# Performance work log

Measured on AMD Instinct MI355X. Metric: run time of the kernel, lower is better.

The kernel has to match this reference:

```python
import jax, jax.numpy as jnp
import numpy as np

N_NODES = 50000
N_EDGES = 800000
N_GRAPHS = 64
IN_CH = 64
HID = 64


def _gcn(x, W, b, src, dst, norm, self_norm, n):
    # GCNConv with self-loops and symmetric normalization (PyG defaults)
    h = x @ W  # [N, H]
    agg = jax.ops.segment_sum(norm[:, None] * h[src], dst, num_segments=n)
    return agg + self_norm[:, None] * h + b


def setup_inputs() -> dict:
    key = jax.random.key(0)
    ks = jax.random.split(key, 20)
    s = 0.1
    d = {
        'x': jax.random.normal(ks[0], (N_NODES, IN_CH), jnp.float32),
        'x_SC': jax.random.normal(ks[1], (N_NODES, IN_CH), jnp.float32),
        'W1': jax.random.normal(ks[2], (IN_CH, HID), jnp.float32) * s,
        'b1': jax.random.normal(ks[3], (HID,), jnp.float32) * s,
        'W2': jax.random.normal(ks[4], (HID, HID), jnp.float32) * s,
        'b2': jax.random.normal(ks[5], (HID,), jnp.float32) * s,
        'We': jax.random.normal(ks[6], (IN_CH, HID), jnp.float32) * s,
        'be': jax.random.normal(ks[7], (HID,), jnp.float32) * s,
        'W1s': jax.random.normal(ks[8], (IN_CH, HID), jnp.float32) * s,
        'b1s': jax.random.normal(ks[9], (HID,), jnp.float32) * s,
        'W2s': jax.random.normal(ks[10], (HID, HID), jnp.float32) * s,
        'b2s': jax.random.normal(ks[11], (HID,), jnp.float32) * s,
        'Wes': jax.random.normal(ks[12], (IN_CH, HID), jnp.float32) * s,
        'bes': jax.random.normal(ks[13], (HID,), jnp.float32) * s,
        'Wf': jax.random.normal(ks[14], (HID, 1), jnp.float32) * s,
        'bf': jax.random.normal(ks[15], (1,), jnp.float32) * s,
        'edge_index': jax.random.randint(ks[16], (2, N_EDGES), 0, N_NODES, jnp.int32),
        'batch': jnp.sort(jax.random.randint(ks[17], (N_NODES,), 0, N_GRAPHS, jnp.int32)),
        'num_graphs': N_GRAPHS,
    }
    return d


def reference(x, x_SC, W1, b1, W2, b2, We, be, W1s, b1s, W2s, b2s, Wes, bes, Wf, bf, edge_index, batch, num_graphs):
    n = x.shape[0]
    src, dst = edge_index[0], edge_index[1]
    # degree with self-loops (edge weight 1)
    deg = jnp.ones((n,), x.dtype).at[dst].add(jnp.ones((src.shape[0],), x.dtype))
    dinv = deg ** -0.5
    norm = dinv[src] * dinv[dst]
    self_norm = dinv * dinv

    h = jax.nn.relu(_gcn(x, W1, b1, src, dst, norm, self_norm, n)) + jax.nn.relu(x @ We + be)
    h = jax.nn.relu(_gcn(h, W2, b2, src, dst, norm, self_norm, n)) + h

    hs = jax.nn.relu(_gcn(x_SC, W1s, b1s, src, dst, norm, self_norm, n)) + jax.nn.relu(x_SC @ Wes + bes)
    hs = jax.nn.relu(_gcn(hs, W2s, b2s, src, dst, norm, self_norm, n)) + hs

    h = h + hs
    sums = jax.ops.segment_sum(h, batch, num_segments=num_graphs)
    cnts = jax.ops.segment_sum(jnp.ones((n,), h.dtype), batch, num_segments=num_graphs)
    pooled = sums / jnp.maximum(cnts, 1.0)[:, None]
    return pooled @ Wf + bf
```

## Files before the change

kernel.cpp:

```cpp
#include <hip/hip_runtime.h>
#include <stdint.h>


typedef _Float16 f16;
typedef _Float16 f16x2 __attribute__((ext_vector_type(2)));
typedef _Float16 f16x8 __attribute__((ext_vector_type(8)));
typedef float f32x4 __attribute__((ext_vector_type(4)));

__global__ void deg_count_k(const int* __restrict__ dst, int nE, int* __restrict__ cnt) {
    int i = blockIdx.x * blockDim.x + threadIdx.x;
    if (i < nE) atomicAdd(&cnt[dst[i]], 1);
}

__global__ void dinv_k(const int* __restrict__ cnt, int n, float* __restrict__ dinv) {
    int i = blockIdx.x * blockDim.x + threadIdx.x;
    if (i < n) dinv[i] = 1.0f / sqrtf(1.0f + (float)cnt[i]);
}

__global__ __launch_bounds__(256) void scanA_k(const int* __restrict__ cnt, int n,
                                               int* __restrict__ offs, int* __restrict__ bsums) {
    int tid = threadIdx.x, lane = tid & 63, wid = tid >> 6;
    int base = blockIdx.x * 1024 + tid * 4;
    int v0 = (base + 0 < n) ? cnt[base + 0] : 0;
    int v1 = (base + 1 < n) ? cnt[base + 1] : 0;
    int v2 = (base + 2 < n) ? cnt[base + 2] : 0;
    int v3 = (base + 3 < n) ? cnt[base + 3] : 0;
    int lsum = v0 + v1 + v2 + v3;
    int s = lsum;
#pragma unroll
    for (int off = 1; off < 64; off <<= 1) {
        int t = __shfl_up(s, off);
        if (lane >= off) s += t;
    }
    __shared__ int wt[4];
    if (lane == 63) wt[wid] = s;
    __syncthreads();
    int woff = 0;
    for (int w = 0; w < wid; ++w) woff += wt[w];
    int excl = woff + s - lsum;
    if (base + 0 < n) offs[base + 0] = excl;
    if (base + 1 < n) offs[base + 1] = excl + v0;
    if (base + 2 < n) offs[base + 2] = excl + v0 + v1;
    if (base + 3 < n) offs[base + 3] = excl + v0 + v1 + v2;
    if (tid == 0) bsums[blockIdx.x] = wt[0] + wt[1] + wt[2] + wt[3];
}

__global__ void scanB_k(const int* __restrict__ bsums, int nb, int* __restrict__ boffs) {
    int lane = threadIdx.x;
    int carry = 0;
    for (int base = 0; base < nb; base += 64) {
        int i = base + lane;
        int v = (i < nb) ? bsums[i] : 0;
        int s = v;
#pragma unroll
        for (int off = 1; off < 64; off <<= 1) {
            int t = __shfl_up(s, off);
            if (lane >= off) s += t;
        }
        if (i < nb) boffs[i] = carry + s - v;
        carry += __shfl(s, 63);
    }
}

__global__ __launch_bounds__(256) void scanC_k(int* __restrict__ offs,
                                               const int* __restrict__ boffs,
                                               int* __restrict__ cur, int n, int nE) {
    int boff = boffs[blockIdx.x];
    int base = blockIdx.x * 1024 + threadIdx.x * 4;
#pragma unroll
    for (int j = 0; j < 4; ++j) {
        int i = base + j;
        if (i < n) {
            int o = offs[i] + boff;
            offs[i] = o;
            cur[i] = o;
        }
    }
    if (blockIdx.x == 0 && threadIdx.x == 0) offs[n] = nE;
}

__global__ void fill_k(const int* __restrict__ src, const int* __restrict__ dst, int nE,
                       int* __restrict__ cur, int* __restrict__ elist) {
    int e = blockIdx.x * blockDim.x + threadIdx.x;
    if (e < nE) {
        int p = atomicAdd(&cur[dst[e]], 1);
        elist[p] = src[e];
    }
}

template <int NW, bool F16IN>
__global__ __launch_bounds__(256) void mm_mfma_k(
    const void* __restrict__ X1, const void* __restrict__ X2,
    const float* __restrict__ Wa1, const float* __restrict__ Wa2,
    const float* __restrict__ Wc1, const float* __restrict__ Wc2,
    const float* __restrict__ dinv,
    f16* __restrict__ Oa1, f16* __restrict__ Oa2,
    f16* __restrict__ Oc1, f16* __restrict__ Oc2,
    int xP, int oP, int n) {
    const int branch = blockIdx.y;
    const void* X   = branch ? X2 : X1;
    const float* Wa = branch ? Wa2 : Wa1;
    const float* Wc = branch ? Wc2 : Wc1;
    f16* Oa = branch ? Oa2 : Oa1;
    f16* Oc = branch ? Oc2 : Oc1;

    const int lane = threadIdx.x & 63;
    const int col = lane & 15;
    const int kgrp = lane >> 4;

    f16x8 wa[4][2], wc[4][2];
#pragma unroll
    for (int ct = 0; ct < 4; ++ct)
#pragma unroll
        for (int kk = 0; kk < 2; ++kk) {
#pragma unroll
            for (int j = 0; j < 8; ++j) {
                int widx = (kk * 32 + kgrp * 8 + j) * 64 + ct * 16 + col;
                wa[ct][kk][j] = (f16)Wa[widx];
                if (NW == 2) wc[ct][kk][j] = (f16)Wc[widx];
            }
        }

    const int wid = blockIdx.x * 4 + (threadIdx.x >> 6);
    const int nwaves = gridDim.x * 4;
    const int ntiles = (n + 15) >> 4;
    for (int t = wid; t < ntiles; t += nwaves) {
        int arow = t * 16 + col;
        if (arow >= n) arow = n - 1;
        f16x8 af[2];
#pragma unroll
        for (int kk = 0; kk < 2; ++kk) {
            if (F16IN) {
                af[kk] = *(const f16x8*)((const f16*)X + (size_t)arow * xP + kk * 32 + kgrp * 8);
            } else {
                const float4* px = (const float4*)((const float*)X + (size_t)arow * xP + kk * 32 + kgrp * 8);
                float4 u0 = px[0], u1 = px[1];
                af[kk][0] = (f16)u0.x; af[kk][1] = (f16)u0.y;
                af[kk][2] = (f16)u0.z; af[kk][3] = (f16)u0.w;
                af[kk][4] = (f16)u1.x; af[kk][5] = (f16)u1.y;
                af[kk][6] = (f16)u1.z; af[kk][7] = (f16)u1.w;
            }
        }
        f32x4 acca[4], accc[4];
#pragma unroll
        for (int ct = 0; ct < 4; ++ct) {
            acca[ct] = (f32x4)(0.0f);
            if (NW == 2) accc[ct] = (f32x4)(0.0f);
        }
#pragma unroll
        for (int ct = 0; ct < 4; ++ct)
#pragma unroll
            for (int kk = 0; kk < 2; ++kk) {
                acca[ct] = __builtin_amdgcn_mfma_f32_16x16x32_f16(af[kk], wa[ct][kk], acca[ct], 0, 0, 0);
                if (NW == 2)
                    accc[ct] = __builtin_amdgcn_mfma_f32_16x16x32_f16(af[kk], wc[ct][kk], accc[ct], 0, 0, 0);
            }
        int rbase = t * 16 + kgrp * 4;
#pragma unroll
        for (int j = 0; j < 4; ++j) {
            int row = rbase + j;
            if (row < n) {
                float d = dinv[row];
#pragma unroll
                for (int ct = 0; ct < 4; ++ct) {
                    Oa[(size_t)row * oP + ct * 16 + col] = (f16)(d * acca[ct][j]);
                    if (NW == 2)
                        Oc[(size_t)row * oP + ct * 16 + col] = (f16)(accc[ct][j]);
                }
            }
        }
    }
}

__global__ __launch_bounds__(256) void agg1_k(
    const int* __restrict__ offs, const int* __restrict__ elist,
    const uint32_t* __restrict__ Aw, const uint32_t* __restrict__ Sw,
    const float* __restrict__ b1, const float* __restrict__ b1s,
    const float* __restrict__ be, const float* __restrict__ bes,
    const float* __restrict__ dinv, uint32_t* __restrict__ Hw, int n) {
    int node = blockIdx.x * 4 + (threadIdx.x >> 6);
    int lane = threadIdx.x & 63;
    if (node >= n) return;
    int br = lane >> 5;
    int ch0 = (lane & 31) * 2;
    float bb0 = br ? b1s[ch0] : b1[ch0];
    float bb1 = br ? b1s[ch0 + 1] : b1[ch0 + 1];
    float bs0 = br ? bes[ch0] : be[ch0];
    float bs1 = br ? bes[ch0 + 1] : be[ch0 + 1];

    int e0 = offs[node], e1 = offs[node + 1];
    f16x2 selfv = __builtin_bit_cast(f16x2, Aw[(size_t)node * 64 + lane]);
    float acc0 = (float)selfv.x, acc1 = (float)selfv.y;
    int e = e0;
    for (; e + 7 < e1; e += 8) {
        int s0 = elist[e], s1 = elist[e + 1], s2 = elist[e + 2], s3 = elist[e + 3];
        int s4 = elist[e + 4], s5 = elist[e + 5], s6 = elist[e + 6], s7 = elist[e + 7];
        f16x2 v0 = __builtin_bit_cast(f16x2, Aw[(size_t)s0 * 64 + lane]);
        f16x2 v1 = __builtin_bit_cast(f16x2, Aw[(size_t)s1 * 64 + lane]);
        f16x2 v2 = __builtin_bit_cast(f16x2, Aw[(size_t)s2 * 64 + lane]);
        f16x2 v3 = __builtin_bit_cast(f16x2, Aw[(size_t)s3 * 64 + lane]);
        f16x2 v4 = __builtin_bit_cast(f16x2, Aw[(size_t)s4 * 64 + lane]);
        f16x2 v5 = __builtin_bit_cast(f16x2, Aw[(size_t)s5 * 64 + lane]);
        f16x2 v6 = __builtin_bit_cast(f16x2, Aw[(size_t)s6 * 64 + lane]);
        f16x2 v7 = __builtin_bit_cast(f16x2, Aw[(size_t)s7 * 64 + lane]);
        acc0 += (((float)v0.x + (float)v1.x) + ((float)v2.x + (float)v3.x)) +
                (((float)v4.x + (float)v5.x) + ((float)v6.x + (float)v7.x));
        acc1 += (((float)v0.y + (float)v1.y) + ((float)v2.y + (float)v3.y)) +
                (((float)v4.y + (float)v5.y) + ((float)v6.y + (float)v7.y));
    }
    for (; e < e1; ++e) {
        f16x2 v = __builtin_bit_cast(f16x2, Aw[(size_t)elist[e] * 64 + lane]);
        acc0 += (float)v.x;
        acc1 += (float)v.y;
    }
    float d = dinv[node];
    float g0 = fmaxf(d * acc0 + bb0, 0.0f);
    float g1 = fmaxf(d * acc1 + bb1, 0.0f);
    f16x2 sv = __builtin_bit_cast(f16x2, Sw[(size_t)node * 64 + lane]);
    g0 += fmaxf((float)sv.x + bs0, 0.0f);
    g1 += fmaxf((float)sv.y + bs1, 0.0f);
    f16x2 o; o.x = (f16)g0; o.y = (f16)g1;
    Hw[(size_t)node * 64 + lane] = __builtin_bit_cast(uint32_t, o);
}

__global__ __launch_bounds__(256) void agg2_dot_k(
    const int* __restrict__ offs, const int* __restrict__ elist,
    const uint32_t* __restrict__ Aw, const uint32_t* __restrict__ Hw,
    const float* __restrict__ b2, const float* __restrict__ b2s,
    const float* __restrict__ Wf, const float* __restrict__ dinv,
    float* __restrict__ dot, int n) {
    int node = blockIdx.x * 4 + (threadIdx.x >> 6);
    int lane = threadIdx.x & 63;
    if (node >= n) return;
    int br = lane >> 5;
    int ch0 = (lane & 31) * 2;
    float bb0 = br ? b2s[ch0] : b2[ch0];
    float bb1 = br ? b2s[ch0 + 1] : b2[ch0 + 1];
    float wf0 = Wf[ch0], wf1 = Wf[ch0 + 1];

    int e0 = offs[node], e1 = offs[node + 1];
    f16x2 selfv = __builtin_bit_cast(f16x2, Aw[(size_t)node * 64 + lane]);
    float acc0 = (float)selfv.x, acc1 = (float)selfv.y;
    int e = e0;
    for (; e + 7 < e1; e += 8) {
        int s0 = elist[e], s1 = elist[e + 1], s2 = elist[e + 2], s3 = elist[e + 3];
        int s4 = elist[e + 4], s5 = elist[e + 5], s6 = elist[e + 6], s7 = elist[e + 7];
        f16x2 v0 = __builtin_bit_cast(f16x2, Aw[(size_t)s0 * 64 + lane]);
        f16x2 v1 = __builtin_bit_cast(f16x2, Aw[(size_t)s1 * 64 + lane]);
        f16x2 v2 = __builtin_bit_cast(f16x2, Aw[(size_t)s2 * 64 + lane]);
        f16x2 v3 = __builtin_bit_cast(f16x2, Aw[(size_t)s3 * 64 + lane]);
        f16x2 v4 = __builtin_bit_cast(f16x2, Aw[(size_t)s4 * 64 + lane]);
        f16x2 v5 = __builtin_bit_cast(f16x2, Aw[(size_t)s5 * 64 + lane]);
        f16x2 v6 = __builtin_bit_cast(f16x2, Aw[(size_t)s6 * 64 + lane]);
        f16x2 v7 = __builtin_bit_cast(f16x2, Aw[(size_t)s7 * 64 + lane]);
        acc0 += (((float)v0.x + (float)v1.x) + ((float)v2.x + (float)v3.x)) +
                (((float)v4.x + (float)v5.x) + ((float)v6.x + (float)v7.x));
        acc1 += (((float)v0.y + (float)v1.y) + ((float)v2.y + (float)v3.y)) +
                (((float)v4.y + (float)v5.y) + ((float)v6.y + (float)v7.y));
    }
    for (; e < e1; ++e) {
        f16x2 v = __builtin_bit_cast(f16x2, Aw[(size_t)elist[e] * 64 + lane]);
        acc0 += (float)v.x;
        acc1 += (float)v.y;
    }
    float d = dinv[node];
    f16x2 hv = __builtin_bit_cast(f16x2, Hw[(size_t)node * 64 + lane]);
    float h0 = fmaxf(d * acc0 + bb0, 0.0f) + (float)hv.x;
    float h1 = fmaxf(d * acc1 + bb1, 0.0f) + (float)hv.y;
    float c = h0 * wf0 + h1 * wf1;
#pragma unroll
    for (int off = 32; off > 0; off >>= 1) c += __shfl_down(c, off);
    if (lane == 0) dot[node] = c;
}

__device__ inline int lower_bound(const int* __restrict__ batch, int n, int g) {
    int lo = 0, hi = n;
    while (lo < hi) {
        int mid = (lo + hi) >> 1;
        if (batch[mid] < g) lo = mid + 1; else hi = mid;
    }
    return lo;
}

__global__ __launch_bounds__(256) void pool_reduce_k(
    const float* __restrict__ dot, const int* __restrict__ batch, int n,
    const float* __restrict__ bf, float* __restrict__ out) {
    int g = blockIdx.x;
    int start = lower_bound(batch, n, g);
    int end = lower_bound(batch, n, g + 1);
    int tid = threadIdx.x, lane = tid & 63, wid = tid >> 6;
    float acc = 0.f;
    for (int i = start + tid; i < end; i += blockDim.x) acc += dot[i];
#pragma unroll
    for (int off = 32; off > 0; off >>= 1) acc += __shfl_down(acc, off);
    __shared__ float part[4];
    if (lane == 0) part[wid] = acc;
    __syncthreads();
    if (tid == 0) {
        float s = part[0] + part[1] + part[2] + part[3];
        float cnt = fmaxf((float)(end - start), 1.0f);
        out[g] = s / cnt + bf[0];
    }
}

static inline char* alignp(char* p, uintptr_t a) {
    return (char*)(((uintptr_t)p + a - 1) & ~(a - 1));
}

extern "C" void kernel_launch(void* const* d_in, const int* in_sizes, int n_in,
                              void* d_out, int out_size, void* d_ws, size_t ws_size,
                              hipStream_t stream) {
    const float* x    = (const float*)d_in[0];
    const float* x_SC = (const float*)d_in[1];
    const float* W1   = (const float*)d_in[2];
    const float* b1   = (const float*)d_in[3];
    const float* W2   = (const float*)d_in[4];
    const float* b2   = (const float*)d_in[5];
    const float* We   = (const float*)d_in[6];
    const float* be   = (const float*)d_in[7];
    const float* W1s  = (const float*)d_in[8];
    const float* b1s  = (const float*)d_in[9];
    const float* W2s  = (const float*)d_in[10];
    const float* b2s  = (const float*)d_in[11];
    const float* Wes  = (const float*)d_in[12];
    const float* bes  = (const float*)d_in[13];
    const float* Wf   = (const float*)d_in[14];
    const float* bf   = (const float*)d_in[15];
    const int* ei     = (const int*)d_in[16];
    const int* batch  = (const int*)d_in[17];

    const int nN = in_sizes[0] / 64;
    const int nE = in_sizes[16] / 2;
    const int nG = out_size;
    const int* esrc = ei;
    const int* edst = ei + nE;
    const int nb = (nN + 1023) / 1024;

    char* p = (char*)d_ws;
    int* cur    = (int*)p;   p = alignp(p + (size_t)nN * sizeof(int), 64);
    int* offs   = (int*)p;   p = alignp(p + (size_t)(nN + 1) * sizeof(int), 64);
    int* elist  = (int*)p;   p = alignp(p + (size_t)nE * sizeof(int), 64);
    int* bsums  = (int*)p;   p = alignp(p + 1024 * sizeof(int), 64);
    int* boffs  = (int*)p;   p = alignp(p + 1024 * sizeof(int), 64);
    float* dinv = (float*)p; p = alignp(p + (size_t)nN * sizeof(float), 64);
    float* dot  = (float*)p; p = alignp(p + (size_t)nN * sizeof(float), 64);
    f16* A = (f16*)p;        p = alignp(p + (size_t)nN * 128 * sizeof(f16), 64);
    f16* S = (f16*)p;        p = alignp(p + (size_t)nN * 128 * sizeof(f16), 64);
    f16* H = (f16*)p;        p = alignp(p + (size_t)nN * 128 * sizeof(f16), 64);

    const int thr = 256;
    const int gEdgeT = (nE + thr - 1) / thr;
    const int gNodeT = (nN + thr - 1) / thr;
    const int gNodeW = (nN + 3) / 4;

    hipMemsetAsync(cur, 0, (size_t)nN * sizeof(int), stream);
    deg_count_k<<<gEdgeT, thr, 0, stream>>>(edst, nE, cur);
    dinv_k<<<gNodeT, thr, 0, stream>>>(cur, nN, dinv);
    scanA_k<<<nb, thr, 0, stream>>>(cur, nN, offs, bsums);
    scanB_k<<<1, 64, 0, stream>>>(bsums, nb, boffs);
    scanC_k<<<nb, thr, 0, stream>>>(offs, boffs, cur, nN, nE);
    fill_k<<<gEdgeT, thr, 0, stream>>>(esrc, edst, nE, cur, elist);

    mm_mfma_k<2, false><<<dim3(256, 2), thr, 0, stream>>>(
        x, x_SC, W1, W1s, We, Wes, dinv,
        A, A + 64, S, S + 64, 64, 128, nN);
    agg1_k<<<gNodeW, thr, 0, stream>>>(offs, elist, (const uint32_t*)A, (const uint32_t*)S,
                                       b1, b1s, be, bes, dinv, (uint32_t*)H, nN);

    mm_mfma_k<1, true><<<dim3(256, 2), thr, 0, stream>>>(
        H, H + 64, W2, W2s, nullptr, nullptr, dinv,
        A, A + 64, nullptr, nullptr, 128, 128, nN);
    agg2_dot_k<<<gNodeW, thr, 0, stream>>>(offs, elist, (const uint32_t*)A, (const uint32_t*)H,
                                           b2, b2s, Wf, dinv, dot, nN);

    pool_reduce_k<<<nG, thr, 0, stream>>>(dot, batch, nN, bf, (float*)d_out);
}
```

Baseline: 319.3 us.

## Fuse preprocessing kernels and merge CSR fill with first matmul launch

Moves the dinv computation into the first scan pass and drops the separate block-offset scan, so each scanC block sums the preceding block totals itself (at most ~49 values). The CSR edge fill and the first dual-weight MFMA matmul now run in one launch, with block ranges split by blockIdx, letting the two independent jobs overlap and saving kernel launches. The second matmul becomes a dedicated, simplified kernel. The trade-off is less launch overhead and serialisation against a few redundant reads in scanC and a fused kernel that mixes very different work.

Result: slower. 329.9 us (+3.3%).

```diff
diff --git a/kernel.cpp b/kernel.cpp
--- a/kernel.cpp
+++ b/kernel.cpp
@@ -12,19 +12,19 @@
     if (i < nE) atomicAdd(&cnt[dst[i]], 1);
 }
 
-__global__ void dinv_k(const int* __restrict__ cnt, int n, float* __restrict__ dinv) {
-    int i = blockIdx.x * blockDim.x + threadIdx.x;
-    if (i < n) dinv[i] = 1.0f / sqrtf(1.0f + (float)cnt[i]);
-}
-
 __global__ __launch_bounds__(256) void scanA_k(const int* __restrict__ cnt, int n,
-                                               int* __restrict__ offs, int* __restrict__ bsums) {
+                                               int* __restrict__ offs, int* __restrict__ bsums,
+                                               float* __restrict__ dinv) {
     int tid = threadIdx.x, lane = tid & 63, wid = tid >> 6;
     int base = blockIdx.x * 1024 + tid * 4;
     int v0 = (base + 0 < n) ? cnt[base + 0] : 0;
     int v1 = (base + 1 < n) ? cnt[base + 1] : 0;
     int v2 = (base + 2 < n) ? cnt[base + 2] : 0;
     int v3 = (base + 3 < n) ? cnt[base + 3] : 0;
+    if (base + 0 < n) dinv[base + 0] = 1.0f / sqrtf(1.0f + (float)v0);
+    if (base + 1 < n) dinv[base + 1] = 1.0f / sqrtf(1.0f + (float)v1);
+    if (base + 2 < n) dinv[base + 2] = 1.0f / sqrtf(1.0f + (float)v2);
+    if (base + 3 < n) dinv[base + 3] = 1.0f / sqrtf(1.0f + (float)v3);
     int lsum = v0 + v1 + v2 + v3;
     int s = lsum;
 #pragma unroll
@@ -45,27 +45,11 @@
     if (tid == 0) bsums[blockIdx.x] = wt[0] + wt[1] + wt[2] + wt[3];
 }
 
-__global__ void scanB_k(const int* __restrict__ bsums, int nb, int* __restrict__ boffs) {
-    int lane = threadIdx.x;
-    int carry = 0;
-    for (int base = 0; base < nb; base += 64) {
-        int i = base + lane;
-        int v = (i < nb) ? bsums[i] : 0;
-        int s = v;
-#pragma unroll
-        for (int off = 1; off < 64; off <<= 1) {
-            int t = __shfl_up(s, off);
-            if (lane >= off) s += t;
-        }
-        if (i < nb) boffs[i] = carry + s - v;
-        carry += __shfl(s, 63);
-    }
-}
-
 __global__ __launch_bounds__(256) void scanC_k(int* __restrict__ offs,
-                                               const int* __restrict__ boffs,
+                                               const int* __restrict__ bsums,
                                                int* __restrict__ cur, int n, int nE) {
-    int boff = boffs[blockIdx.x];
+    int boff = 0;
+    for (int b = 0; b < (int)blockIdx.x; ++b) boff += bsums[b];
     int base = blockIdx.x * 1024 + threadIdx.x * 4;
 #pragma unroll
     for (int j = 0; j < 4; ++j) {
@@ -79,30 +63,30 @@
     if (blockIdx.x == 0 && threadIdx.x == 0) offs[n] = nE;
 }
 
-__global__ void fill_k(const int* __restrict__ src, const int* __restrict__ dst, int nE,
-                       int* __restrict__ cur, int* __restrict__ elist) {
-    int e = blockIdx.x * blockDim.x + threadIdx.x;
-    if (e < nE) {
-        int p = atomicAdd(&cur[dst[e]], 1);
-        elist[p] = src[e];
-    }
-}
-
-template <int NW, bool F16IN>
-__global__ __launch_bounds__(256) void mm_mfma_k(
-    const void* __restrict__ X1, const void* __restrict__ X2,
+__global__ __launch_bounds__(256) void fillmm_k(
+    const int* __restrict__ src, const int* __restrict__ dst, int nE,
+    int* __restrict__ cur, int* __restrict__ elist, int nFill,
+    const float* __restrict__ X1, const float* __restrict__ X2,
     const float* __restrict__ Wa1, const float* __restrict__ Wa2,
     const float* __restrict__ Wc1, const float* __restrict__ Wc2,
     const float* __restrict__ dinv,
-    f16* __restrict__ Oa1, f16* __restrict__ Oa2,
-    f16* __restrict__ Oc1, f16* __restrict__ Oc2,
-    int xP, int oP, int n) {
-    const int branch = blockIdx.y;
-    const void* X   = branch ? X2 : X1;
+    f16* __restrict__ A, f16* __restrict__ S, int n) {
+    if ((int)blockIdx.x < nFill) {
+        int e = blockIdx.x * blockDim.x + threadIdx.x;
+        if (e < nE) {
+            int p = atomicAdd(&cur[dst[e]], 1);
+            elist[p] = src[e];
+        }
+        return;
+    }
+    const int bid = blockIdx.x - nFill;
+    const int branch = bid >> 8;
+    const int bx = bid & 255;
+    const float* X  = branch ? X2 : X1;
     const float* Wa = branch ? Wa2 : Wa1;
     const float* Wc = branch ? Wc2 : Wc1;
-    f16* Oa = branch ? Oa2 : Oa1;
-    f16* Oc = branch ? Oc2 : Oc1;
+    f16* Oa = A + branch * 64;
+    f16* Oc = S + branch * 64;
 
     const int lane = threadIdx.x & 63;
     const int col = lane & 15;
@@ -117,7 +101,77 @@
             for (int j = 0; j < 8; ++j) {
                 int widx = (kk * 32 + kgrp * 8 + j) * 64 + ct * 16 + col;
                 wa[ct][kk][j] = (f16)Wa[widx];
-                if (NW == 2) wc[ct][kk][j] = (f16)Wc[widx];
+                wc[ct][kk][j] = (f16)Wc[widx];
+            }
+        }
+
+    const int wid = bx * 4 + (threadIdx.x >> 6);
+    const int nwaves = 256 * 4;
+    const int ntiles = (n + 15) >> 4;
+    for (int t = wid; t < ntiles; t += nwaves) {
+        int arow = t * 16 + col;
+        if (arow >= n) arow = n - 1;
+        f16x8 af[2];
+#pragma unroll
+        for (int kk = 0; kk < 2; ++kk) {
+            const float4* px = (const float4*)(X + (size_t)arow * 64 + kk * 32 + kgrp * 8);
+            float4 u0 = px[0], u1 = px[1];
+            af[kk][0] = (f16)u0.x; af[kk][1] = (f16)u0.y;
+            af[kk][2] = (f16)u0.z; af[kk][3] = (f16)u0.w;
+            af[kk][4] = (f16)u1.x; af[kk][5] = (f16)u1.y;
+            af[kk][6] = (f16)u1.z; af[kk][7] = (f16)u1.w;
+        }
+        f32x4 acca[4], accc[4];
+#pragma unroll
+        for (int ct = 0; ct < 4; ++ct) {
+            acca[ct] = (f32x4)(0.0f);
+            accc[ct] = (f32x4)(0.0f);
+        }
+#pragma unroll
+        for (int ct = 0; ct < 4; ++ct)
+#pragma unroll
+            for (int kk = 0; kk < 2; ++kk) {
+                acca[ct] = __builtin_amdgcn_mfma_f32_16x16x32_f16(af[kk], wa[ct][kk], acca[ct], 0, 0, 0);
+                accc[ct] = __builtin_amdgcn_mfma_f32_16x16x32_f16(af[kk], wc[ct][kk], accc[ct], 0, 0, 0);
+            }
+        int rbase = t * 16 + kgrp * 4;
+#pragma unroll
+        for (int j = 0; j < 4; ++j) {
+            int row = rbase + j;
+            if (row < n) {
+                float d = dinv[row];
+#pragma unroll
+                for (int ct = 0; ct < 4; ++ct) {
+                    Oa[(size_t)row * 128 + ct * 16 + col] = (f16)(d * acca[ct][j]);
+                    Oc[(size_t)row * 128 + ct * 16 + col] = (f16)(accc[ct][j]);
+                }
+            }
+        }
+    }
+}
+
+__global__ __launch_bounds__(256) void mm2_k(
+    const f16* __restrict__ H,
+    const float* __restrict__ Wa1, const float* __restrict__ Wa2,
+    const float* __restrict__ dinv, f16* __restrict__ A, int n) {
+    const int branch = blockIdx.y;
+    const float* Wa = branch ? Wa2 : Wa1;
+    const f16* X = H + branch * 64;
+    f16* Oa = A + branch * 64;
+
+    const int lane = threadIdx.x & 63;
+    const int col = lane & 15;
+    const int kgrp = lane >> 4;
+
+    f16x8 wa[4][2];
+#pragma unroll
+    for (int ct = 0; ct < 4; ++ct)
+#pragma unroll
+        for (int kk = 0; kk < 2; ++kk) {
+#pragma unroll
+            for (int j = 0; j < 8; ++j) {
+                int widx = (kk * 32 + kgrp * 8 + j) * 64 + ct * 16 + col;
+                wa[ct][kk][j] = (f16)Wa[widx];
             }
         }
 
@@ -129,32 +183,16 @@
         if (arow >= n) arow = n - 1;
         f16x8 af[2];
 #pragma unroll
-        for (int kk = 0; kk < 2; ++kk) {
-            if (F16IN) {
-                af[kk] = *(const f16x8*)((const f16*)X + (size_t)arow * xP + kk * 32 + kgrp * 8);
-            } else {
-                const float4* px = (const float4*)((const float*)X + (size_t)arow * xP + kk * 32 + kgrp * 8);
-                float4 u0 = px[0], u1 = px[1];
-                af[kk][0] = (f16)u0.x; af[kk][1] = (f16)u0.y;
-                af[kk][2] = (f16)u0.z; af[kk][3] = (f16)u0.w;
-                af[kk][4] = (f16)u1.x; af[kk][5] = (f16)u1.y;
-                af[kk][6] = (f16)u1.z; af[kk][7] = (f16)u1.w;
-            }
-        }
-        f32x4 acca[4], accc[4];
-#pragma unroll
-        for (int ct = 0; ct < 4; ++ct) {
-            acca[ct] = (f32x4)(0.0f);
-            if (NW == 2) accc[ct] = (f32x4)(0.0f);
-        }
+        for (int kk = 0; kk < 2; ++kk)
+            af[kk] = *(const f16x8*)(X + (size_t)arow * 128 + kk * 32 + kgrp * 8);
+        f32x4 acca[4];
+#pragma unroll
+        for (int ct = 0; ct < 4; ++ct) acca[ct] = (f32x4)(0.0f);
 #pragma unroll
         for (int ct = 0; ct < 4; ++ct)
 #pragma unroll
-            for (int kk = 0; kk < 2; ++kk) {
+            for (int kk = 0; kk < 2; ++kk)
                 acca[ct] = __builtin_amdgcn_mfma_f32_16x16x32_f16(af[kk], wa[ct][kk], acca[ct], 0, 0, 0);
-                if (NW == 2)
-                    accc[ct] = __builtin_amdgcn_mfma_f32_16x16x32_f16(af[kk], wc[ct][kk], accc[ct], 0, 0, 0);
-            }
         int rbase = t * 16 + kgrp * 4;
 #pragma unroll
         for (int j = 0; j < 4; ++j) {
@@ -162,11 +200,8 @@
             if (row < n) {
                 float d = dinv[row];
 #pragma unroll
-                for (int ct = 0; ct < 4; ++ct) {
-                    Oa[(size_t)row * oP + ct * 16 + col] = (f16)(d * acca[ct][j]);
-                    if (NW == 2)
-                        Oc[(size_t)row * oP + ct * 16 + col] = (f16)(accc[ct][j]);
-                }
+                for (int ct = 0; ct < 4; ++ct)
+                    Oa[(size_t)row * 128 + ct * 16 + col] = (f16)(d * acca[ct][j]);
             }
         }
     }
@@ -341,7 +376,6 @@
     int* offs   = (int*)p;   p = alignp(p + (size_t)(nN + 1) * sizeof(int), 64);
     int* elist  = (int*)p;   p = alignp(p + (size_t)nE * sizeof(int), 64);
     int* bsums  = (int*)p;   p = alignp(p + 1024 * sizeof(int), 64);
-    int* boffs  = (int*)p;   p = alignp(p + 1024 * sizeof(int), 64);
     float* dinv = (float*)p; p = alignp(p + (size_t)nN * sizeof(float), 64);
     float* dot  = (float*)p; p = alignp(p + (size_t)nN * sizeof(float), 64);
     f16* A = (f16*)p;        p = alignp(p + (size_t)nN * 128 * sizeof(f16), 64);
@@ -350,26 +384,21 @@
 
     const int thr = 256;
     const int gEdgeT = (nE + thr - 1) / thr;
-    const int gNodeT = (nN + thr - 1) / thr;
     const int gNodeW = (nN + 3) / 4;
 
     hipMemsetAsync(cur, 0, (size_t)nN * sizeof(int), stream);
     deg_count_k<<<gEdgeT, thr, 0, stream>>>(edst, nE, cur);
-    dinv_k<<<gNodeT, thr, 0, stream>>>(cur, nN, dinv);
-    scanA_k<<<nb, thr, 0, stream>>>(cur, nN, offs, bsums);
-    scanB_k<<<1, 64, 0, stream>>>(bsums, nb, boffs);
-    scanC_k<<<nb, thr, 0, stream>>>(offs, boffs, cur, nN, nE);
-    fill_k<<<gEdgeT, thr, 0, stream>>>(esrc, edst, nE, cur, elist);
-
-    mm_mfma_k<2, false><<<dim3(256, 2), thr, 0, stream>>>(
-        x, x_SC, W1, W1s, We, Wes, dinv,
-        A, A + 64, S, S + 64, 64, 128, nN);
+    scanA_k<<<nb, thr, 0, stream>>>(cur, nN, offs, bsums, dinv);
+    scanC_k<<<nb, thr, 0, stream>>>(offs, bsums, cur, nN, nE);
+
+    fillmm_k<<<gEdgeT + 512, thr, 0, stream>>>(
+        esrc, edst, nE, cur, elist, gEdgeT,
+        x, x_SC, W1, W1s, We, Wes, dinv, A, S, nN);
+
     agg1_k<<<gNodeW, thr, 0, stream>>>(offs, elist, (const uint32_t*)A, (const uint32_t*)S,
                                        b1, b1s, be, bes, dinv, (uint32_t*)H, nN);
 
-    mm_mfma_k<1, true><<<dim3(256, 2), thr, 0, stream>>>(
-        H, H + 64, W2, W2s, nullptr, nullptr, dinv,
-        A, A + 64, nullptr, nullptr, 128, 128, nN);
+    mm2_k<<<dim3(256, 2), thr, 0, stream>>>(H, W2, W2s, dinv, A, nN);
     agg2_dot_k<<<gNodeW, thr, 0, stream>>>(offs, elist, (const uint32_t*)A, (const uint32_t*)H,
                                            b2, b2s, Wf, dinv, dot, nN);
 
```

## Fuse the whole GCN pipeline into one persistent cooperative kernel

Applied to the files above, without the earlier changes.

Replaces the dozen separate launches (memset, degree count, three-stage scan, CSR fill, two matmuls, two aggregations, pooling) with one cooperative kernel whose stages are separated by grid-wide barriers. The CSR build now records each edge's rank from the degree-count atomic, so the fill pass needs no second atomic. The edge fill is also overlapped with the first matmul stage before the next barrier. This removes launch gaps and tail idle time between kernels, at the cost of about ten grid syncs and a fixed persistent grid size that may limit occupancy in the gather-heavy stages.

Measured after the change: 945.6 us. +196.2%, slower.

```diff
diff --git a/kernel.cpp b/kernel.cpp
--- a/kernel.cpp
+++ b/kernel.cpp
@@ -1,5 +1,8 @@
 #include <hip/hip_runtime.h>
+#include <hip/hip_cooperative_groups.h>
 #include <stdint.h>
+
+namespace cg = cooperative_groups;
 
 
 typedef _Float16 f16;
@@ -7,122 +10,44 @@
 typedef _Float16 f16x8 __attribute__((ext_vector_type(8)));
 typedef float f32x4 __attribute__((ext_vector_type(4)));
 
-__global__ void deg_count_k(const int* __restrict__ dst, int nE, int* __restrict__ cnt) {
-    int i = blockIdx.x * blockDim.x + threadIdx.x;
-    if (i < nE) atomicAdd(&cnt[dst[i]], 1);
-}
-
-__global__ void dinv_k(const int* __restrict__ cnt, int n, float* __restrict__ dinv) {
-    int i = blockIdx.x * blockDim.x + threadIdx.x;
-    if (i < n) dinv[i] = 1.0f / sqrtf(1.0f + (float)cnt[i]);
-}
-
-__global__ __launch_bounds__(256) void scanA_k(const int* __restrict__ cnt, int n,
-                                               int* __restrict__ offs, int* __restrict__ bsums) {
-    int tid = threadIdx.x, lane = tid & 63, wid = tid >> 6;
-    int base = blockIdx.x * 1024 + tid * 4;
-    int v0 = (base + 0 < n) ? cnt[base + 0] : 0;
-    int v1 = (base + 1 < n) ? cnt[base + 1] : 0;
-    int v2 = (base + 2 < n) ? cnt[base + 2] : 0;
-    int v3 = (base + 3 < n) ? cnt[base + 3] : 0;
-    int lsum = v0 + v1 + v2 + v3;
-    int s = lsum;
-#pragma unroll
-    for (int off = 1; off < 64; off <<= 1) {
-        int t = __shfl_up(s, off);
-        if (lane >= off) s += t;
-    }
-    __shared__ int wt[4];
-    if (lane == 63) wt[wid] = s;
-    __syncthreads();
-    int woff = 0;
-    for (int w = 0; w < wid; ++w) woff += wt[w];
-    int excl = woff + s - lsum;
-    if (base + 0 < n) offs[base + 0] = excl;
-    if (base + 1 < n) offs[base + 1] = excl + v0;
-    if (base + 2 < n) offs[base + 2] = excl + v0 + v1;
-    if (base + 3 < n) offs[base + 3] = excl + v0 + v1 + v2;
-    if (tid == 0) bsums[blockIdx.x] = wt[0] + wt[1] + wt[2] + wt[3];
-}
-
-__global__ void scanB_k(const int* __restrict__ bsums, int nb, int* __restrict__ boffs) {
-    int lane = threadIdx.x;
-    int carry = 0;
-    for (int base = 0; base < nb; base += 64) {
-        int i = base + lane;
-        int v = (i < nb) ? bsums[i] : 0;
-        int s = v;
-#pragma unroll
-        for (int off = 1; off < 64; off <<= 1) {
-            int t = __shfl_up(s, off);
-            if (lane >= off) s += t;
-        }
-        if (i < nb) boffs[i] = carry + s - v;
-        carry += __shfl(s, 63);
-    }
-}
-
-__global__ __launch_bounds__(256) void scanC_k(int* __restrict__ offs,
-                                               const int* __restrict__ boffs,
-                                               int* __restrict__ cur, int n, int nE) {
-    int boff = boffs[blockIdx.x];
-    int base = blockIdx.x * 1024 + threadIdx.x * 4;
-#pragma unroll
-    for (int j = 0; j < 4; ++j) {
-        int i = base + j;
-        if (i < n) {
-            int o = offs[i] + boff;
-            offs[i] = o;
-            cur[i] = o;
-        }
-    }
-    if (blockIdx.x == 0 && threadIdx.x == 0) offs[n] = nE;
-}
-
-__global__ void fill_k(const int* __restrict__ src, const int* __restrict__ dst, int nE,
-                       int* __restrict__ cur, int* __restrict__ elist) {
-    int e = blockIdx.x * blockDim.x + threadIdx.x;
-    if (e < nE) {
-        int p = atomicAdd(&cur[dst[e]], 1);
-        elist[p] = src[e];
-    }
-}
-
-template <int NW, bool F16IN>
-__global__ __launch_bounds__(256) void mm_mfma_k(
-    const void* __restrict__ X1, const void* __restrict__ X2,
-    const float* __restrict__ Wa1, const float* __restrict__ Wa2,
-    const float* __restrict__ Wc1, const float* __restrict__ Wc2,
-    const float* __restrict__ dinv,
-    f16* __restrict__ Oa1, f16* __restrict__ Oa2,
-    f16* __restrict__ Oc1, f16* __restrict__ Oc2,
-    int xP, int oP, int n) {
-    const int branch = blockIdx.y;
-    const void* X   = branch ? X2 : X1;
-    const float* Wa = branch ? Wa2 : Wa1;
-    const float* Wc = branch ? Wc2 : Wc1;
-    f16* Oa = branch ? Oa2 : Oa1;
-    f16* Oc = branch ? Oc2 : Oc1;
-
-    const int lane = threadIdx.x & 63;
-    const int col = lane & 15;
-    const int kgrp = lane >> 4;
-
+struct Args {
+    const int* esrc; const int* edst;
+    const float* x; const float* xsc;
+    const float *W1, *b1, *W2, *b2, *We, *be;
+    const float *W1s, *b1s, *W2s, *b2s, *Wes, *bes;
+    const float *Wf, *bf;
+    const int* batch;
+    int* cnt; int* rank_; int* offs; int* bsums; int* elist;
+    float* dinv; float* dot;
+    f16 *A, *S, *H;
+    float* out;
+    int nN, nE, nG;
+};
+
+__device__ inline int lower_bound_d(const int* __restrict__ b, int n, int g) {
+    int lo = 0, hi = n;
+    while (lo < hi) { int m = (lo + hi) >> 1; if (b[m] < g) lo = m + 1; else hi = m; }
+    return lo;
+}
+
+template <bool F16IN, bool HASC>
+__device__ void mm_dev(const void* __restrict__ Xv,
+                       const float* __restrict__ Wa, const float* __restrict__ Wc,
+                       const float* __restrict__ dinv,
+                       f16* __restrict__ Oa, f16* __restrict__ Oc,
+                       int n, int xP, int wid, int nwaves, int lane) {
+    const int col = lane & 15, kgrp = lane >> 4;
     f16x8 wa[4][2], wc[4][2];
 #pragma unroll
     for (int ct = 0; ct < 4; ++ct)
 #pragma unroll
-        for (int kk = 0; kk < 2; ++kk) {
+        for (int kk = 0; kk < 2; ++kk)
 #pragma unroll
             for (int j = 0; j < 8; ++j) {
                 int widx = (kk * 32 + kgrp * 8 + j) * 64 + ct * 16 + col;
                 wa[ct][kk][j] = (f16)Wa[widx];
-                if (NW == 2) wc[ct][kk][j] = (f16)Wc[widx];
-            }
-        }
-
-    const int wid = blockIdx.x * 4 + (threadIdx.x >> 6);
-    const int nwaves = gridDim.x * 4;
+                if (HASC) wc[ct][kk][j] = (f16)Wc[widx];
+            }
     const int ntiles = (n + 15) >> 4;
     for (int t = wid; t < ntiles; t += nwaves) {
         int arow = t * 16 + col;
@@ -131,9 +56,9 @@
 #pragma unroll
         for (int kk = 0; kk < 2; ++kk) {
             if (F16IN) {
-                af[kk] = *(const f16x8*)((const f16*)X + (size_t)arow * xP + kk * 32 + kgrp * 8);
+                af[kk] = *(const f16x8*)((const f16*)Xv + (size_t)arow * xP + kk * 32 + kgrp * 8);
             } else {
-                const float4* px = (const float4*)((const float*)X + (size_t)arow * xP + kk * 32 + kgrp * 8);
+                const float4* px = (const float4*)((const float*)Xv + (size_t)arow * xP + kk * 32 + kgrp * 8);
                 float4 u0 = px[0], u1 = px[1];
                 af[kk][0] = (f16)u0.x; af[kk][1] = (f16)u0.y;
                 af[kk][2] = (f16)u0.z; af[kk][3] = (f16)u0.w;
@@ -145,15 +70,14 @@
 #pragma unroll
         for (int ct = 0; ct < 4; ++ct) {
             acca[ct] = (f32x4)(0.0f);
-            if (NW == 2) accc[ct] = (f32x4)(0.0f);
+            if (HASC) accc[ct] = (f32x4)(0.0f);
         }
 #pragma unroll
         for (int ct = 0; ct < 4; ++ct)
 #pragma unroll
             for (int kk = 0; kk < 2; ++kk) {
                 acca[ct] = __builtin_amdgcn_mfma_f32_16x16x32_f16(af[kk], wa[ct][kk], acca[ct], 0, 0, 0);
-                if (NW == 2)
-                    accc[ct] = __builtin_amdgcn_mfma_f32_16x16x32_f16(af[kk], wc[ct][kk], accc[ct], 0, 0, 0);
+                if (HASC) accc[ct] = __builtin_amdgcn_mfma_f32_16x16x32_f16(af[kk], wc[ct][kk], accc[ct], 0, 0, 0);
             }
         int rbase = t * 16 + kgrp * 4;
 #pragma unroll
@@ -163,215 +87,242 @@
                 float d = dinv[row];
 #pragma unroll
                 for (int ct = 0; ct < 4; ++ct) {
-                    Oa[(size_t)row * oP + ct * 16 + col] = (f16)(d * acca[ct][j]);
-                    if (NW == 2)
-                        Oc[(size_t)row * oP + ct * 16 + col] = (f16)(accc[ct][j]);
+                    Oa[(size_t)row * 128 + ct * 16 + col] = (f16)(d * acca[ct][j]);
+                    if (HASC) Oc[(size_t)row * 128 + ct * 16 + col] = (f16)(accc[ct][j]);
                 }
             }
         }
     }
 }
 
-__global__ __launch_bounds__(256) void agg1_k(
-    const int* __restrict__ offs, const int* __restrict__ elist,
-    const uint32_t* __restrict__ Aw, const uint32_t* __restrict__ Sw,
-    const float* __restrict__ b1, const float* __restrict__ b1s,
-    const float* __restrict__ be, const float* __restrict__ bes,
-    const float* __restrict__ dinv, uint32_t* __restrict__ Hw, int n) {
-    int node = blockIdx.x * 4 + (threadIdx.x >> 6);
-    int lane = threadIdx.x & 63;
-    if (node >= n) return;
-    int br = lane >> 5;
-    int ch0 = (lane & 31) * 2;
-    float bb0 = br ? b1s[ch0] : b1[ch0];
-    float bb1 = br ? b1s[ch0 + 1] : b1[ch0 + 1];
-    float bs0 = br ? bes[ch0] : be[ch0];
-    float bs1 = br ? bes[ch0 + 1] : be[ch0 + 1];
-
-    int e0 = offs[node], e1 = offs[node + 1];
-    f16x2 selfv = __builtin_bit_cast(f16x2, Aw[(size_t)node * 64 + lane]);
-    float acc0 = (float)selfv.x, acc1 = (float)selfv.y;
-    int e = e0;
-    for (; e + 7 < e1; e += 8) {
-        int s0 = elist[e], s1 = elist[e + 1], s2 = elist[e + 2], s3 = elist[e + 3];
-        int s4 = elist[e + 4], s5 = elist[e + 5], s6 = elist[e + 6], s7 = elist[e + 7];
-        f16x2 v0 = __builtin_bit_cast(f16x2, Aw[(size_t)s0 * 64 + lane]);
-        f16x2 v1 = __builtin_bit_cast(f16x2, Aw[(size_t)s1 * 64 + lane]);
-        f16x2 v2 = __builtin_bit_cast(f16x2, Aw[(size_t)s2 * 64 + lane]);
-        f16x2 v3 = __builtin_bit_cast(f16x2, Aw[(size_t)s3 * 64 + lane]);
-        f16x2 v4 = __builtin_bit_cast(f16x2, Aw[(size_t)s4 * 64 + lane]);
-        f16x2 v5 = __builtin_bit_cast(f16x2, Aw[(size_t)s5 * 64 + lane]);
-        f16x2 v6 = __builtin_bit_cast(f16x2, Aw[(size_t)s6 * 64 + lane]);
-        f16x2 v7 = __builtin_bit_cast(f16x2, Aw[(size_t)s7 * 64 + lane]);
-        acc0 += (((float)v0.x + (float)v1.x) + ((float)v2.x + (float)v3.x)) +
-                (((float)v4.x + (float)v5.x) + ((float)v6.x + (float)v7.x));
-        acc1 += (((float)v0.y + (float)v1.y) + ((float)v2.y + (float)v3.y)) +
-                (((float)v4.y + (float)v5.y) + ((float)v6.y + (float)v7.y));
-    }
-    for (; e < e1; ++e) {
-        f16x2 v = __builtin_bit_cast(f16x2, Aw[(size_t)elist[e] * 64 + lane]);
-        acc0 += (float)v.x;
-        acc1 += (float)v.y;
-    }
-    float d = dinv[node];
-    float g0 = fmaxf(d * acc0 + bb0, 0.0f);
-    float g1 = fmaxf(d * acc1 + bb1, 0.0f);
-    f16x2 sv = __builtin_bit_cast(f16x2, Sw[(size_t)node * 64 + lane]);
-    g0 += fmaxf((float)sv.x + bs0, 0.0f);
-    g1 += fmaxf((float)sv.y + bs1, 0.0f);
-    f16x2 o; o.x = (f16)g0; o.y = (f16)g1;
-    Hw[(size_t)node * 64 + lane] = __builtin_bit_cast(uint32_t, o);
-}
-
-__global__ __launch_bounds__(256) void agg2_dot_k(
-    const int* __restrict__ offs, const int* __restrict__ elist,
-    const uint32_t* __restrict__ Aw, const uint32_t* __restrict__ Hw,
-    const float* __restrict__ b2, const float* __restrict__ b2s,
-    const float* __restrict__ Wf, const float* __restrict__ dinv,
-    float* __restrict__ dot, int n) {
-    int node = blockIdx.x * 4 + (threadIdx.x >> 6);
-    int lane = threadIdx.x & 63;
-    if (node >= n) return;
-    int br = lane >> 5;
-    int ch0 = (lane & 31) * 2;
-    float bb0 = br ? b2s[ch0] : b2[ch0];
-    float bb1 = br ? b2s[ch0 + 1] : b2[ch0 + 1];
-    float wf0 = Wf[ch0], wf1 = Wf[ch0 + 1];
-
-    int e0 = offs[node], e1 = offs[node + 1];
-    f16x2 selfv = __builtin_bit_cast(f16x2, Aw[(size_t)node * 64 + lane]);
-    float acc0 = (float)selfv.x, acc1 = (float)selfv.y;
-    int e = e0;
-    for (; e + 7 < e1; e += 8) {
-        int s0 = elist[e], s1 = elist[e + 1], s2 = elist[e + 2], s3 = elist[e + 3];
-        int s4 = elist[e + 4], s5 = elist[e + 5], s6 = elist[e + 6], s7 = elist[e + 7];
-        f16x2 v0 = __builtin_bit_cast(f16x2, Aw[(size_t)s0 * 64 + lane]);
-        f16x2 v1 = __builtin_bit_cast(f16x2, Aw[(size_t)s1 * 64 + lane]);
-        f16x2 v2 = __builtin_bit_cast(f16x2, Aw[(size_t)s2 * 64 + lane]);
-        f16x2 v3 = __builtin_bit_cast(f16x2, Aw[(size_t)s3 * 64 + lane]);
-        f16x2 v4 = __builtin_bit_cast(f16x2, Aw[(size_t)s4 * 64 + lane]);
-        f16x2 v5 = __builtin_bit_cast(f16x2, Aw[(size_t)s5 * 64 + lane]);
-        f16x2 v6 = __builtin_bit_cast(f16x2, Aw[(size_t)s6 * 64 + lane]);
-        f16x2 v7 = __builtin_bit_cast(f16x2, Aw[(size_t)s7 * 64 + lane]);
-        acc0 += (((float)v0.x + (float)v1.x) + ((float)v2.x + (float)v3.x)) +
-                (((float)v4.x + (float)v5.x) + ((float)v6.x + (float)v7.x));
-        acc1 += (((float)v0.y + (float)v1.y) + ((float)v2.y + (float)v3.y)) +
-                (((float)v4.y + (float)v5.y) + ((float)v6.y + (float)v7.y));
-    }
-    for (; e < e1; ++e) {
-        f16x2 v = __builtin_bit_cast(f16x2, Aw[(size_t)elist[e] * 64 + lane]);
-        acc0 += (float)v.x;
-        acc1 += (float)v.y;
-    }
-    float d = dinv[node];
-    f16x2 hv = __builtin_bit_cast(f16x2, Hw[(size_t)node * 64 + lane]);
-    float h0 = fmaxf(d * acc0 + bb0, 0.0f) + (float)hv.x;
-    float h1 = fmaxf(d * acc1 + bb1, 0.0f) + (float)hv.y;
-    float c = h0 * wf0 + h1 * wf1;
-#pragma unroll
-    for (int off = 32; off > 0; off >>= 1) c += __shfl_down(c, off);
-    if (lane == 0) dot[node] = c;
-}
-
-__device__ inline int lower_bound(const int* __restrict__ batch, int n, int g) {
-    int lo = 0, hi = n;
-    while (lo < hi) {
-        int mid = (lo + hi) >> 1;
-        if (batch[mid] < g) lo = mid + 1; else hi = mid;
-    }
-    return lo;
-}
-
-__global__ __launch_bounds__(256) void pool_reduce_k(
-    const float* __restrict__ dot, const int* __restrict__ batch, int n,
-    const float* __restrict__ bf, float* __restrict__ out) {
-    int g = blockIdx.x;
-    int start = lower_bound(batch, n, g);
-    int end = lower_bound(batch, n, g + 1);
-    int tid = threadIdx.x, lane = tid & 63, wid = tid >> 6;
-    float acc = 0.f;
-    for (int i = start + tid; i < end; i += blockDim.x) acc += dot[i];
-#pragma unroll
-    for (int off = 32; off > 0; off >>= 1) acc += __shfl_down(acc, off);
-    __shared__ float part[4];
-    if (lane == 0) part[wid] = acc;
-    __syncthreads();
-    if (tid == 0) {
-        float s = part[0] + part[1] + part[2] + part[3];
-        float cnt = fmaxf((float)(end - start), 1.0f);
-        out[g] = s / cnt + bf[0];
-    }
-}
-
-static inline char* alignp(char* p, uintptr_t a) {
-    return (char*)(((uintptr_t)p + a - 1) & ~(a - 1));
+__global__ __launch_bounds__(256, 4) void fused_k(Args a) {
+    cg::grid_group grid = cg::this_grid();
+    const int tid = threadIdx.x;
+    const int lane = tid & 63;
+    const int gtid = blockIdx.x * 256 + tid;
+    const int gstride = gridDim.x * 256;
+    const int wid = blockIdx.x * 4 + (tid >> 6);
+    const int nwaves = gridDim.x * 4;
+
+    for (int i = gtid; i < a.nN; i += gstride) a.cnt[i] = 0;
+    grid.sync();
+
+    for (int e = gtid; e < a.nE; e += gstride)
+        a.rank_[e] = atomicAdd(&a.cnt[a.edst[e]], 1);
+    grid.sync();
+
+    const int C = (a.nN + gridDim.x - 1) / gridDim.x;
+    if (tid < 64) {
+        int base = blockIdx.x * C;
+        int carry = 0;
+        for (int s0 = 0; s0 < C; s0 += 64) {
+            int idx = s0 + tid;
+            int i = base + idx;
+            bool ok = (idx < C) && (i < a.nN);
+            int v = ok ? a.cnt[i] : 0;
+            if (ok) a.dinv[i] = 1.0f / sqrtf(1.0f + (float)v);
+            int s = v;
+#pragma unroll
+            for (int off = 1; off < 64; off <<= 1) { int t = __shfl_up(s, off); if (lane >= off) s += t; }
+            if (ok) a.offs[i] = carry + s - v;
+            carry += __shfl(s, 63);
+        }
+        if (tid == 0) a.bsums[blockIdx.x] = carry;
+    }
+    grid.sync();
+
+    if (blockIdx.x == 0 && tid < 64) {
+        int carry = 0;
+        for (int b0 = 0; b0 < (int)gridDim.x; b0 += 64) {
+            int i = b0 + tid;
+            int v = (i < (int)gridDim.x) ? a.bsums[i] : 0;
+            int s = v;
+#pragma unroll
+            for (int off = 1; off < 64; off <<= 1) { int t = __shfl_up(s, off); if (lane >= off) s += t; }
+            if (i < (int)gridDim.x) a.bsums[i] = carry + s - v;
+            carry += __shfl(s, 63);
+        }
+    }
+    grid.sync();
+
+    {
+        int boff = a.bsums[blockIdx.x];
+        for (int j = tid; j < C; j += 256) {
+            int i = blockIdx.x * C + j;
+            if (i < a.nN) a.offs[i] += boff;
+        }
+        if (gtid == 0) a.offs[a.nN] = a.nE;
+    }
+    grid.sync();
+
+    for (int e = gtid; e < a.nE; e += gstride)
+        a.elist[a.offs[a.edst[e]] + a.rank_[e]] = a.esrc[e];
+    mm_dev<false, true>(a.x,   a.W1,  a.We,  a.dinv, a.A,      a.S,      a.nN, 64, wid, nwaves, lane);
+    mm_dev<false, true>(a.xsc, a.W1s, a.Wes, a.dinv, a.A + 64, a.S + 64, a.nN, 64, wid, nwaves, lane);
+    grid.sync();
+
+    {
+        const uint32_t* Aw = (const uint32_t*)a.A;
+        const uint32_t* Sw = (const uint32_t*)a.S;
+        uint32_t* Hw = (uint32_t*)a.H;
+        int br = lane >> 5;
+        int ch0 = (lane & 31) * 2;
+        float bb0 = br ? a.b1s[ch0] : a.b1[ch0];
+        float bb1 = br ? a.b1s[ch0 + 1] : a.b1[ch0 + 1];
+        float bs0 = br ? a.bes[ch0] : a.be[ch0];
+        float bs1 = br ? a.bes[ch0 + 1] : a.be[ch0 + 1];
+        for (int node = wid; node < a.nN; node += nwaves) {
+            int e0 = a.offs[node], e1 = a.offs[node + 1];
+            f16x2 sv = __builtin_bit_cast(f16x2, Aw[(size_t)node * 64 + lane]);
+            float acc0 = (float)sv.x, acc1 = (float)sv.y;
+            int e = e0;
+            for (; e + 7 < e1; e += 8) {
+                int s0 = a.elist[e],     s1 = a.elist[e + 1], s2 = a.elist[e + 2], s3 = a.elist[e + 3];
+                int s4 = a.elist[e + 4], s5 = a.elist[e + 5], s6 = a.elist[e + 6], s7 = a.elist[e + 7];
+                f16x2 v0 = __builtin_bit_cast(f16x2, Aw[(size_t)s0 * 64 + lane]);
+                f16x2 v1 = __builtin_bit_cast(f16x2, Aw[(size_t)s1 * 64 + lane]);
+                f16x2 v2 = __builtin_bit_cast(f16x2, Aw[(size_t)s2 * 64 + lane]);
+                f16x2 v3 = __builtin_bit_cast(f16x2, Aw[(size_t)s3 * 64 + lane]);
+                f16x2 v4 = __builtin_bit_cast(f16x2, Aw[(size_t)s4 * 64 + lane]);
+                f16x2 v5 = __builtin_bit_cast(f16x2, Aw[(size_t)s5 * 64 + lane]);
+                f16x2 v6 = __builtin_bit_cast(f16x2, Aw[(size_t)s6 * 64 + lane]);
+                f16x2 v7 = __builtin_bit_cast(f16x2, Aw[(size_t)s7 * 64 + lane]);
+                acc0 += (((float)v0.x + (float)v1.x) + ((float)v2.x + (float)v3.x)) +
+                        (((float)v4.x + (float)v5.x) + ((float)v6.x + (float)v7.x));
+                acc1 += (((float)v0.y + (float)v1.y) + ((float)v2.y + (float)v3.y)) +
+                        (((float)v4.y + (float)v5.y) + ((float)v6.y + (float)v7.y));
+            }
+            for (; e < e1; ++e) {
+                f16x2 v = __builtin_bit_cast(f16x2, Aw[(size_t)a.elist[e] * 64 + lane]);
+                acc0 += (float)v.x; acc1 += (float)v.y;
+            }
+            float d = a.dinv[node];
+            float g0 = fmaxf(d * acc0 + bb0, 0.0f);
+            float g1 = fmaxf(d * acc1 + bb1, 0.0f);
+            f16x2 skv = __builtin_bit_cast(f16x2, Sw[(size_t)node * 64 + lane]);
+            g0 += fmaxf((float)skv.x + bs0, 0.0f);
+            g1 += fmaxf((float)skv.y + bs1, 0.0f);
+            f16x2 o; o.x = (f16)g0; o.y = (f16)g1;
+            Hw[(size_t)node * 64 + lane] = __builtin_bit_cast(uint32_t, o);
+        }
+    }
+    grid.sync();
+
+    mm_dev<true, false>(a.H,      a.W2,  nullptr, a.dinv, a.A,      nullptr, a.nN, 128, wid, nwaves, lane);
+    mm_dev<true, false>(a.H + 64, a.W2s, nullptr, a.dinv, a.A + 64, nullptr, a.nN, 128, wid, nwaves, lane);
+    grid.sync();
+
+    {
+        const uint32_t* Aw = (const uint32_t*)a.A;
+        const uint32_t* Hw = (const uint32_t*)a.H;
+        int br = lane >> 5;
+        int ch0 = (lane & 31) * 2;
+        float bb0 = br ? a.b2s[ch0] : a.b2[ch0];
+        float bb1 = br ? a.b2s[ch0 + 1] : a.b2[ch0 + 1];
+        float wf0 = a.Wf[ch0], wf1 = a.Wf[ch0 + 1];
+        for (int node = wid; node < a.nN; node += nwaves) {
+            int e0 = a.offs[node], e1 = a.offs[node + 1];
+            f16x2 sv = __builtin_bit_cast(f16x2, Aw[(size_t)node * 64 + lane]);
+            float acc0 = (float)sv.x, acc1 = (float)sv.y;
+            int e = e0;
+            for (; e + 7 < e1; e += 8) {
+                int s0 = a.elist[e],     s1 = a.elist[e + 1], s2 = a.elist[e + 2], s3 = a.elist[e + 3];
+                int s4 = a.elist[e + 4], s5 = a.elist[e + 5], s6 = a.elist[e + 6], s7 = a.elist[e + 7];
+                f16x2 v0 = __builtin_bit_cast(f16x2, Aw[(size_t)s0 * 64 + lane]);
+                f16x2 v1 = __builtin_bit_cast(f16x2, Aw[(size_t)s1 * 64 + lane]);
+                f16x2 v2 = __builtin_bit_cast(f16x2, Aw[(size_t)s2 * 64 + lane]);
+                f16x2 v3 = __builtin_bit_cast(f16x2, Aw[(size_t)s3 * 64 + lane]);
+                f16x2 v4 = __builtin_bit_cast(f16x2, Aw[(size_t)s4 * 64 + lane]);
+                f16x2 v5 = __builtin_bit_cast(f16x2, Aw[(size_t)s5 * 64 + lane]);
+                f16x2 v6 = __builtin_bit_cast(f16x2, Aw[(size_t)s6 * 64 + lane]);
+                f16x2 v7 = __builtin_bit_cast(f16x2, Aw[(size_t)s7 * 64 + lane]);
+                acc0 += (((float)v0.x + (float)v1.x) + ((float)v2.x + (float)v3.x)) +
+                        (((float)v4.x + (float)v5.x) + ((float)v6.x + (float)v7.x));
+                acc1 += (((float)v0.y + (float)v1.y) + ((float)v2.y + (float)v3.y)) +
+                        (((float)v4.y + (float)v5.y) + ((float)v6.y + (float)v7.y));
+            }
+            for (; e < e1; ++e) {
+                f16x2 v = __builtin_bit_cast(f16x2, Aw[(size_t)a.elist[e] * 64 + lane]);
+                acc0 += (float)v.x; acc1 += (float)v.y;
+            }
+            float d = a.dinv[node];
+            f16x2 hv = __builtin_bit_cast(f16x2, Hw[(size_t)node * 64 + lane]);
+            float h0 = fmaxf(d * acc0 + bb0, 0.0f) + (float)hv.x;
+            float h1 = fmaxf(d * acc1 + bb1, 0.0f) + (float)hv.y;
+            float c = h0 * wf0 + h1 * wf1;
+#pragma unroll
+            for (int off = 32; off > 0; off >>= 1) c += __shfl_down(c, off);
+            if (lane == 0) a.dot[node] = c;
+        }
+    }
+    grid.sync();
+
+    if ((int)blockIdx.x < a.nG) {
+        int g = blockIdx.x;
+        int start = lower_bound_d(a.batch, a.nN, g);
+        int end   = lower_bound_d(a.batch, a.nN, g + 1);
+        float acc = 0.0f;
+        for (int i = start + tid; i < end; i += 256) acc += a.dot[i];
+#pragma unroll
+        for (int off = 32; off > 0; off >>= 1) acc += __shfl_down(acc, off);
+        __shared__ float part[4];
+        if (lane == 0) part[tid >> 6] = acc;
+        __syncthreads();
+        if (tid == 0) {
+            float s = part[0] + part[1] + part[2] + part[3];
+            float c = fmaxf((float)(end - start), 1.0f);
+            a.out[g] = s / c + a.bf[0];
+        }
+    }
+}
+
+static inline char* alignp(char* p, uintptr_t al) {
+    return (char*)(((uintptr_t)p + al - 1) & ~(al - 1));
 }
 
 extern "C" void kernel_launch(void* const* d_in, const int* in_sizes, int n_in,
                               void* d_out, int out_size, void* d_ws, size_t ws_size,
                               hipStream_t stream) {
-    const float* x    = (const float*)d_in[0];
-    const float* x_SC = (const float*)d_in[1];
-    const float* W1   = (const float*)d_in[2];
-    const float* b1   = (const float*)d_in[3];
-    const float* W2   = (const float*)d_in[4];
-    const float* b2   = (const float*)d_in[5];
-    const float* We   = (const float*)d_in[6];
-    const float* be   = (const float*)d_in[7];
-    const float* W1s  = (const float*)d_in[8];
-    const float* b1s  = (const float*)d_in[9];
-    const float* W2s  = (const float*)d_in[10];
-    const float* b2s  = (const float*)d_in[11];
-    const float* Wes  = (const float*)d_in[12];
-    const float* bes  = (const float*)d_in[13];
-    const float* Wf   = (const float*)d_in[14];
-    const float* bf   = (const float*)d_in[15];
-    const int* ei     = (const int*)d_in[16];
-    const int* batch  = (const int*)d_in[17];
-
     const int nN = in_sizes[0] / 64;
     const int nE = in_sizes[16] / 2;
     const int nG = out_size;
-    const int* esrc = ei;
-    const int* edst = ei + nE;
-    const int nb = (nN + 1023) / 1024;
+    const int* ei = (const int*)d_in[16];
 
     char* p = (char*)d_ws;
-    int* cur    = (int*)p;   p = alignp(p + (size_t)nN * sizeof(int), 64);
+    int* cnt    = (int*)p;   p = alignp(p + (size_t)nN * sizeof(int), 64);
+    int* rank_  = (int*)p;   p = alignp(p + (size_t)nE * sizeof(int), 64);
     int* offs   = (int*)p;   p = alignp(p + (size_t)(nN + 1) * sizeof(int), 64);
+    int* bsums  = (int*)p;   p = alignp(p + 1024 * sizeof(int), 64);
     int* elist  = (int*)p;   p = alignp(p + (size_t)nE * sizeof(int), 64);
-    int* bsums  = (int*)p;   p = alignp(p + 1024 * sizeof(int), 64);
-    int* boffs  = (int*)p;   p = alignp(p + 1024 * sizeof(int), 64);
     float* dinv = (float*)p; p = alignp(p + (size_t)nN * sizeof(float), 64);
     float* dot  = (float*)p; p = alignp(p + (size_t)nN * sizeof(float), 64);
     f16* A = (f16*)p;        p = alignp(p + (size_t)nN * 128 * sizeof(f16), 64);
     f16* S = (f16*)p;        p = alignp(p + (size_t)nN * 128 * sizeof(f16), 64);
     f16* H = (f16*)p;        p = alignp(p + (size_t)nN * 128 * sizeof(f16), 64);
 
-    const int thr = 256;
-    const int gEdgeT = (nE + thr - 1) / thr;
-    const int gNodeT = (nN + thr - 1) / thr;
-    const int gNodeW = (nN + 3) / 4;
-
-    hipMemsetAsync(cur, 0, (size_t)nN * sizeof(int), stream);
-    deg_count_k<<<gEdgeT, thr, 0, stream>>>(edst, nE, cur);
-    dinv_k<<<gNodeT, thr, 0, stream>>>(cur, nN, dinv);
-    scanA_k<<<nb, thr, 0, stream>>>(cur, nN, offs, bsums);
-    scanB_k<<<1, 64, 0, stream>>>(bsums, nb, boffs);
-    scanC_k<<<nb, thr, 0, stream>>>(offs, boffs, cur, nN, nE);
-    fill_k<<<gEdgeT, thr, 0, stream>>>(esrc, edst, nE, cur, elist);
-
-    mm_mfma_k<2, false><<<dim3(256, 2), thr, 0, stream>>>(
-        x, x_SC, W1, W1s, We, Wes, dinv,
-        A, A + 64, S, S + 64, 64, 128, nN);
-    agg1_k<<<gNodeW, thr, 0, stream>>>(offs, elist, (const uint32_t*)A, (const uint32_t*)S,
-                                       b1, b1s, be, bes, dinv, (uint32_t*)H, nN);
-
-    mm_mfma_k<1, true><<<dim3(256, 2), thr, 0, stream>>>(
-        H, H + 64, W2, W2s, nullptr, nullptr, dinv,
-        A, A + 64, nullptr, nullptr, 128, 128, nN);
-    agg2_dot_k<<<gNodeW, thr, 0, stream>>>(offs, elist, (const uint32_t*)A, (const uint32_t*)H,
-                                           b2, b2s, Wf, dinv, dot, nN);
-
-    pool_reduce_k<<<nG, thr, 0, stream>>>(dot, batch, nN, bf, (float*)d_out);
-}
+    Args a;
+    a.esrc = ei; a.edst = ei + nE;
+    a.x   = (const float*)d_in[0];  a.xsc = (const float*)d_in[1];
+    a.W1  = (const float*)d_in[2];  a.b1  = (const float*)d_in[3];
+    a.W2  = (const float*)d_in[4];  a.b2  = (const float*)d_in[5];
+    a.We  = (const float*)d_in[6];  a.be  = (const float*)d_in[7];
+    a.W1s = (const float*)d_in[8];  a.b1s = (const float*)d_in[9];
+    a.W2s = (const float*)d_in[10]; a.b2s = (const float*)d_in[11];
+    a.Wes = (const float*)d_in[12]; a.bes = (const float*)d_in[13];
+    a.Wf  = (const float*)d_in[14]; a.bf  = (const float*)d_in[15];
+    a.batch = (const int*)d_in[17];
+    a.cnt = cnt; a.rank_ = rank_; a.offs = offs; a.bsums = bsums; a.elist = elist;
+    a.dinv = dinv; a.dot = dot;
+    a.A = A; a.S = S; a.H = H;
+    a.out = (float*)d_out;
+    a.nN = nN; a.nE = nE; a.nG = nG;
+
+    int maxB = 4;
+    hipOccupancyMaxActiveBlocksPerMultiprocessor(&maxB, fused_k, 256, 0);
+    int nBlk = maxB * 256;
+    if (nBlk > 1024) nBlk = 1024;
+    if (nBlk < 64) nBlk = 64;
+
+    void* params[] = { (void*)&a };
+    hipLaunchCooperativeKernel(fused_k, dim3(nBlk), dim3(256), params, 0, stream);
+}
```
